# Optimization experiments

Hardware: AMD Instinct MI355X
Metric: run time of the kernel (lower is better)

Reference implementation:

```python
import jax, jax.numpy as jnp
import numpy as np

B, N, E, H, R, L, VOCAB, KINDS = 8, 4096, 524288, 128, 8, 2, 100000, 8


def setup_inputs() -> dict:
    key = jax.random.key(0)
    ks = jax.random.split(key, 12)
    concept_ids = jax.random.randint(ks[0], (B, N), 1, VOCAB)  # avoid padding_idx 0
    kind_ids = jax.random.randint(ks[1], (B, N), 0, KINDS)
    node_mask = jnp.ones((B, N), dtype=jnp.int32)
    # edges constrained within each batch block (module assumes per-subgraph edges)
    e_batch = jax.random.randint(ks[2], (E,), 0, B)
    src = e_batch * N + jax.random.randint(ks[3], (E,), 0, N)
    dst = e_batch * N + jax.random.randint(ks[4], (E,), 0, N)
    edge_index = jnp.stack([src, dst], axis=0)
    edge_type = jax.random.randint(ks[5], (E,), 0, R)
    s = 0.02
    concept_emb = jax.random.normal(ks[6], (VOCAB, H), jnp.float32) * s
    concept_emb = concept_emb.at[0].set(0.0)  # padding_idx=0
    kind_emb = jax.random.normal(ks[7], (KINDS, H), jnp.float32) * s
    proj_W = jax.random.normal(ks[8], (H, H), jnp.float32) * s
    proj_b = jnp.zeros((H,), jnp.float32)
    self_W = jax.random.normal(ks[9], (L, H, H), jnp.float32) * s
    self_b = jnp.zeros((L, H), jnp.float32)
    rel_W = jax.random.normal(ks[10], (L, R, H, H), jnp.float32) * s
    return dict(pkg_node_concept_ids=concept_ids, pkg_node_kind_ids=kind_ids,
                pkg_node_mask=node_mask, pkg_edge_index=edge_index,
                pkg_edge_type=edge_type, concept_emb=concept_emb, kind_emb=kind_emb,
                proj_W=proj_W, proj_b=proj_b, self_W=self_W, self_b=self_b, rel_W=rel_W)


def reference(pkg_node_concept_ids, pkg_node_kind_ids, pkg_node_mask,
              pkg_edge_index, pkg_edge_type, concept_emb, kind_emb,
              proj_W, proj_b, self_W, self_b, rel_W):
    b, n = pkg_node_concept_ids.shape
    num_nodes = b * n
    # input embedding + projection (dropout = identity in eval)
    x = concept_emb[pkg_node_concept_ids] + kind_emb[pkg_node_kind_ids]  # [B,N,H]
    x = jnp.einsum('bnh,gh->bng', x, proj_W) + proj_b
    x = x.reshape(num_nodes, -1)  # packed node states [B*N, H]
    src, dst = pkg_edge_index[0], pkg_edge_index[1]
    deg = jax.ops.segment_sum(jnp.ones_like(src, dtype=x.dtype), dst,
                              num_segments=num_nodes)[:, None]
    deg = jnp.maximum(deg, 1.0)
    n_layers, n_rel = rel_W.shape[0], rel_W.shape[1]
    for l in range(n_layers):
        xs = x[src]  # [E,H] gather
        msgs = jnp.zeros_like(xs)
        for r in range(n_rel):
            msgs = msgs + jnp.where((pkg_edge_type == r)[:, None],
                                    xs @ rel_W[l, r].T, 0.0)
        agg = jax.ops.segment_sum(msgs, dst, num_segments=num_nodes) / deg
        x = jax.nn.relu(x @ self_W[l].T + self_b[l] + agg)
    out = x.reshape(b, n, -1) * pkg_node_mask[..., None].astype(x.dtype)
    return out
```

## Files before the change

kernel.cpp:

```cpp
#include <hip/hip_runtime.h>
#include <hip/hip_bf16.h>

#define NODES 32768
#define HD 128
#define NE 524288
#define NR 8

typedef unsigned int u32;
typedef unsigned short u16;
typedef __attribute__((ext_vector_type(8))) short bf16x8;
typedef __attribute__((ext_vector_type(4))) float f32x4;

#define XH_OFF   (0u)
#define XL_OFF   (8u<<20)
#define Y_OFF    (16u<<20)
#define Z_OFF    (80u<<20)
#define ADJ_OFF  (96u<<20)
#define RP_OFF   (98u<<20)
#define CUR_OFF  ((98u<<20)+(256u<<10))
#define BSUM_OFF ((98u<<20)+(512u<<10))
#define BP_OFF   ((98u<<20)+(640u<<10))

#define BP_LAYER 294912

__device__ __forceinline__ float bflo(u32 u){ union{u32 i;float f;}c; c.i=u<<16; return c.f; }
__device__ __forceinline__ float bfhi(u32 u){ union{u32 i;float f;}c; c.i=u&0xffff0000u; return c.f; }
__device__ __forceinline__ u16 f2bf(float f){
  u32 u=__float_as_uint(f);
  u32 r=u + 0x7fffu + ((u>>16)&1u);
  return (u16)(r>>16);
}
__device__ __forceinline__ float bf2f(u16 h){ return __uint_as_float(((u32)h)<<16); }

__device__ __forceinline__ void gl_lds16(const void* g, void* l){
  __builtin_amdgcn_global_load_lds((const __attribute__((address_space(1))) u32*)g,
                                   (__attribute__((address_space(3))) u32*)l, 16, 0, 0);
}

__device__ __forceinline__ void fma64(const float* At, const float* Wt,
                                      int mq, int gq, float acc[8][4])
{
#pragma unroll 8
  for(int kk=0;kk<64;kk++){
    const float4 a0=*(const float4*)&At[kk*68+mq*8];
    const float4 a1=*(const float4*)&At[kk*68+mq*8+4];
    const float4 w =*(const float4*)&Wt[kk*132+gq*4];
    float av[8]={a0.x,a0.y,a0.z,a0.w,a1.x,a1.y,a1.z,a1.w};
#pragma unroll
    for(int i=0;i<8;i++){
      acc[i][0]=fmaf(av[i],w.x,acc[i][0]);
      acc[i][1]=fmaf(av[i],w.y,acc[i][1]);
      acc[i][2]=fmaf(av[i],w.z,acc[i][2]);
      acc[i][3]=fmaf(av[i],w.w,acc[i][3]);
    }
  }
}

__global__ __launch_bounds__(256) void embed_gemm(
    const int* __restrict__ cid, const int* __restrict__ kid,
    const float* __restrict__ cemb, const float* __restrict__ kemb,
    const float* __restrict__ pW, const float* __restrict__ pb,
    u16* __restrict__ xh, u16* __restrict__ xl)
{
  __shared__ float At[64*68];
  __shared__ float Wt[64*132];
  const int tid=threadIdx.x;
  const int d0=blockIdx.x*64;
  const int mq=tid>>5, gq=tid&31;
  float acc[8][4];
#pragma unroll
  for(int i=0;i<8;i++){ acc[i][0]=0.f; acc[i][1]=0.f; acc[i][2]=0.f; acc[i][3]=0.f; }

  for(int c=0;c<2;c++){
    const int h0=c*64;
    __syncthreads();
    { int m=tid>>2; int hh=(tid&3)*16;
      int ci=cid[d0+m], ki=kid[d0+m];
      const float* cp=cemb+(size_t)ci*HD+h0+hh;
      const float* kp=kemb+(size_t)ki*HD+h0+hh;
      float* ap=&At[hh*68+m];
#pragma unroll
      for(int j=0;j<16;j+=4){
        float4 a=*(const float4*)(cp+j);
        float4 b=*(const float4*)(kp+j);
        ap[(j+0)*68]=a.x+b.x; ap[(j+1)*68]=a.y+b.y;
        ap[(j+2)*68]=a.z+b.z; ap[(j+3)*68]=a.w+b.w;
      }
    }
    { int g=tid>>1; int hh=(tid&1)*32;
      const float* wp=pW+(size_t)g*HD+h0+hh;
      float* wl=&Wt[hh*132+g];
#pragma unroll
      for(int j=0;j<32;j+=4){
        float4 w=*(const float4*)(wp+j);
        wl[(j+0)*132]=w.x; wl[(j+1)*132]=w.y; wl[(j+2)*132]=w.z; wl[(j+3)*132]=w.w;
      }
    }
    __syncthreads();
    fma64(At,Wt,mq,gq,acc);
  }
  const float4 bias=*(const float4*)&pb[gq*4];
#pragma unroll
  for(int i=0;i<8;i++){
    int m=d0+mq*8+i;
    float v[4]={acc[i][0]+bias.x,acc[i][1]+bias.y,acc[i][2]+bias.z,acc[i][3]+bias.w};
    u16 hb[4], lb[4];
#pragma unroll
    for(int j=0;j<4;j++){ hb[j]=f2bf(v[j]); lb[j]=f2bf(v[j]-bf2f(hb[j])); }
    uint2 hv={(u32)hb[0]|((u32)hb[1]<<16),(u32)hb[2]|((u32)hb[3]<<16)};
    uint2 lv={(u32)lb[0]|((u32)lb[1]<<16),(u32)lb[2]|((u32)lb[3]<<16)};
    *(uint2*)&xh[(size_t)m*HD+gq*4]=hv;
    *(uint2*)&xl[(size_t)m*HD+gq*4]=lv;
  }
}

__global__ void prep_w(const float* __restrict__ rW, const float* __restrict__ sW,
                       u16* __restrict__ Bp)
{
  int idx=blockIdx.x*256+threadIdx.x;
  int l=idx/147456;
  int rem=idx%147456;
  int t=rem>>14;
  int kn=rem&16383;
  int k=kn>>7, n=kn&127;
  float w;
  if(t<8) w=rW[(((size_t)l*NR+t)*HD+n)*HD+k];
  else    w=sW[((size_t)l*HD+n)*HD+k];
  u16* base=Bp+(size_t)l*BP_LAYER+(size_t)t*32768;
  int kc=k>>6, kin=k&63, ks=kin>>5, q=(kin>>3)&3, j=kin&7;
  size_t off=((size_t)(kc*2+ks)*128+n)*32+q*8+j;
  u16 hb=f2bf(w);
  u16 lb=f2bf(w-bf2f(hb));
  base[off]=hb;
  base[off+16384]=lb;
}

__global__ void count_deg(const int* __restrict__ dst, u32* __restrict__ cnt){
  int e=blockIdx.x*256+threadIdx.x;
  atomicAdd(&cnt[dst[e]],1u);
}

__global__ void scan1(const u32* __restrict__ cnt, u32* __restrict__ rp, u32* __restrict__ bsum){
  __shared__ u32 sh[256];
  int t=threadIdx.x; int base=blockIdx.x*256;
  u32 v=cnt[base+t]; sh[t]=v; __syncthreads();
  for(int off=1;off<256;off<<=1){
    u32 tv=(t>=off)?sh[t-off]:0u; __syncthreads();
    sh[t]+=tv; __syncthreads();
  }
  rp[base+t]=sh[t]-v;
  if(t==255) bsum[blockIdx.x]=sh[255];
}

__global__ void scan2(u32* __restrict__ bsum, u32* __restrict__ rp){
  __shared__ u32 sh[128];
  int t=threadIdx.x;
  u32 v=bsum[t]; sh[t]=v; __syncthreads();
  for(int off=1;off<128;off<<=1){
    u32 tv=(t>=off)?sh[t-off]:0u; __syncthreads();
    sh[t]+=tv; __syncthreads();
  }
  bsum[t]=sh[t]-v;
  if(t==0) rp[NODES]=NE;
}

__global__ void scan3(u32* __restrict__ rp, const u32* __restrict__ bsum){
  int i=blockIdx.x*256+threadIdx.x;
  rp[i]+=bsum[blockIdx.x];
}

__global__ void scatter_edges(const int* __restrict__ src, const int* __restrict__ dst,
                              const int* __restrict__ et, const u32* __restrict__ rp,
                              u32* __restrict__ cur, u32* __restrict__ adj){
  int e=blockIdx.x*256+threadIdx.x;
  int d=dst[e];
  u32 pos=atomicAdd(&cur[d],1u);
  adj[rp[d]+pos]=(u32)src[e] | ((u32)et[e]<<16);
}

__global__ __launch_bounds__(256) void gemm_y(
    const u16* __restrict__ xhi, const u16* __restrict__ xlo,
    const u16* __restrict__ Bt, u16* __restrict__ y, float* __restrict__ z)
{
  __shared__ u16 Atile[128*64];
  const int tid=threadIdx.x;
  const int wave=tid>>6, lane=tid&63;
  const int wm=wave>>1, wn=wave&1;
  const int q=lane>>4;
  const int d0=blockIdx.x*128;
  const int t=blockIdx.y;
  const u16* Btile=Bt+(size_t)t*32768;

  f32x4 acc[4][4];
#pragma unroll
  for(int a=0;a<4;a++)
#pragma unroll
    for(int b=0;b<4;b++) acc[a][b]=(f32x4){0.f,0.f,0.f,0.f};

  const int st_row_in = lane>>3;
  const int st_gj = (lane&7) ^ (lane>>3);

#pragma unroll
  for(int part=0;part<2;part++){
    const u16* xs = part? xlo : xhi;
    const int nseg = part? 1 : 2;
    for(int c=0;c<2;c++){
      __syncthreads();
#pragma unroll
      for(int i_=0;i_<4;i_++){
        int r_=wave*32+i_*8+st_row_in;
        const u16* g_=xs+(size_t)(d0+r_)*HD+c*64+st_gj*8;
        gl_lds16(g_, &Atile[(wave*32+i_*8)*64]);
      }
      __syncthreads();
      bf16x8 afr[2][4];
#pragma unroll
      for(int ks=0;ks<2;ks++)
#pragma unroll
        for(int tm=0;tm<4;tm++){
          int m=wm*64+tm*16+(lane&15);
          afr[ks][tm]=*(const bf16x8*)&Atile[m*64+(((ks*4)+q)^(m&7))*8];
        }
      for(int s=0;s<nseg;s++){
        const u16* Bb=Btile + s*16384;
#pragma unroll
        for(int ks=0;ks<2;ks++){
#pragma unroll
          for(int tn=0;tn<4;tn++){
            int n=wn*64+tn*16+(lane&15);
            bf16x8 bfr=*(const bf16x8*)&Bb[((size_t)(c*2+ks)*128+n)*32+q*8];
#pragma unroll
            for(int tm=0;tm<4;tm++)
              acc[tm][tn]=__builtin_amdgcn_mfma_f32_16x16x32_bf16(afr[ks][tm],bfr,acc[tm][tn],0,0,0);
          }
        }
      }
    }
  }

#pragma unroll
  for(int tn=0;tn<4;tn++){
    int n=wn*64+tn*16+(lane&15);
#pragma unroll
    for(int tm=0;tm<4;tm++){
      int rbase=d0+wm*64+tm*16+q*4;
#pragma unroll
      for(int r=0;r<4;r++){
        int m=rbase+r;
        if(t<8) y[((size_t)t*NODES+m)*HD+n]=f2bf(acc[tm][tn][r]);
        else    z[(size_t)m*HD+n]=acc[tm][tn][r];
      }
    }
  }
}

__global__ __launch_bounds__(256) void gather_combine(
    const u32* __restrict__ y, const float* __restrict__ z,
    const u32* __restrict__ adj, const u32* __restrict__ rp,
    const float* __restrict__ sb, const int* __restrict__ mask,
    u32* __restrict__ xh, u32* __restrict__ xl, float* __restrict__ outf, int last)
{
  const int wave=threadIdx.x>>6, lane=threadIdx.x&63;
  const int node=blockIdx.x*4+wave;
  const int beg=(int)rp[node], end=(int)rp[node+1];
  float a0=0.f, a1=0.f;
  int e=beg;
  for(; e+4<=end; e+=4){
    u32 q0=adj[e], q1=adj[e+1], q2=adj[e+2], q3=adj[e+3];
    u32 v0=y[((size_t)(q0>>16)*NODES+(q0&0x7fffu))*64+lane];
    u32 v1=y[((size_t)(q1>>16)*NODES+(q1&0x7fffu))*64+lane];
    u32 v2=y[((size_t)(q2>>16)*NODES+(q2&0x7fffu))*64+lane];
    u32 v3=y[((size_t)(q3>>16)*NODES+(q3&0x7fffu))*64+lane];
    a0+=bflo(v0)+bflo(v1)+bflo(v2)+bflo(v3);
    a1+=bfhi(v0)+bfhi(v1)+bfhi(v2)+bfhi(v3);
  }
  for(; e<end; ++e){
    u32 qq=adj[e];
    u32 v=y[((size_t)(qq>>16)*NODES+(qq&0x7fffu))*64+lane];
    a0+=bflo(v); a1+=bfhi(v);
  }
  float inv=1.f/fmaxf((float)(end-beg),1.f);
  float2 zz=*(const float2*)&z[(size_t)node*HD+2*lane];
  float2 bb=*(const float2*)&sb[2*lane];
  float v0=fmaxf(zz.x+a0*inv+bb.x,0.f);
  float v1=fmaxf(zz.y+a1*inv+bb.y,0.f);
  if(last){
    float mk=(float)mask[node];
    float2 o={v0*mk,v1*mk};
    *(float2*)&outf[(size_t)node*HD+2*lane]=o;
  } else {
    u16 h0=f2bf(v0), h1=f2bf(v1);
    u16 l0=f2bf(v0-bf2f(h0)), l1=f2bf(v1-bf2f(h1));
    xh[(size_t)node*64+lane]=(u32)h0|((u32)h1<<16);
    xl[(size_t)node*64+lane]=(u32)l0|((u32)l1<<16);
  }
}

extern "C" void kernel_launch(void* const* d_in, const int* in_sizes, int n_in,
                              void* d_out, int out_size, void* d_ws, size_t ws_size,
                              hipStream_t stream)
{
  (void)in_sizes; (void)n_in; (void)out_size; (void)ws_size;
  const int*   cid =(const int*)  d_in[0];
  const int*   kid =(const int*)  d_in[1];
  const int*   mask=(const int*)  d_in[2];
  const int*   ei  =(const int*)  d_in[3];
  const int*   et  =(const int*)  d_in[4];
  const float* cemb=(const float*)d_in[5];
  const float* kemb=(const float*)d_in[6];
  const float* pW  =(const float*)d_in[7];
  const float* pb  =(const float*)d_in[8];
  const float* sW  =(const float*)d_in[9];
  const float* sb  =(const float*)d_in[10];
  const float* rW  =(const float*)d_in[11];
  float* out=(float*)d_out;
  char*  ws =(char*)d_ws;

  u16* xh =(u16*)(ws+XH_OFF);
  u16* xl =(u16*)(ws+XL_OFF);
  u16* y  =(u16*)(ws+Y_OFF);
  float* z=(float*)(ws+Z_OFF);
  u32* adj =(u32*)(ws+ADJ_OFF);
  u32* rp  =(u32*)(ws+RP_OFF);
  u32* cur =(u32*)(ws+CUR_OFF);
  u32* bsum=(u32*)(ws+BSUM_OFF);
  u16* Bp  =(u16*)(ws+BP_OFF);
  const int* srcA=ei;
  const int* dstA=ei+NE;

  hipMemsetAsync(cur,0,NODES*sizeof(u32),stream);
  prep_w<<<1152,256,0,stream>>>(rW,sW,Bp);
  embed_gemm<<<NODES/64,256,0,stream>>>(cid,kid,cemb,kemb,pW,pb,xh,xl);
  count_deg<<<NE/256,256,0,stream>>>(dstA,cur);
  scan1<<<NODES/256,256,0,stream>>>(cur,rp,bsum);
  scan2<<<1,128,0,stream>>>(bsum,rp);
  scan3<<<NODES/256,256,0,stream>>>(rp,bsum);
  hipMemsetAsync(cur,0,NODES*sizeof(u32),stream);
  scatter_edges<<<NE/256,256,0,stream>>>(srcA,dstA,et,rp,cur,adj);

  gemm_y<<<dim3(NODES/128,9),256,0,stream>>>(xh,xl,Bp,y,z);
  gather_combine<<<NODES/4,256,0,stream>>>((const u32*)y,z,adj,rp,sb,mask,(u32*)xh,(u32*)xl,out,0);
  gemm_y<<<dim3(NODES/128,9),256,0,stream>>>(xh,xl,Bp+BP_LAYER,y,z);
  gather_combine<<<NODES/4,256,0,stream>>>((const u32*)y,z,adj,rp,sb+HD,mask,(u32*)xh,(u32*)xl,out,1);
}
```

Baseline: 360.9 us.

## Load node tile once and loop all relation transforms inside gemm_y

```diff
diff --git a/kernel.cpp b/kernel.cpp
--- a/kernel.cpp
+++ b/kernel.cpp
@@ -178,77 +178,112 @@
   adj[rp[d]+pos]=(u32)src[e] | ((u32)et[e]<<16);
 }
 
-__global__ __launch_bounds__(256) void gemm_y(
+__global__ __launch_bounds__(256,2) void gemm_y(
     const u16* __restrict__ xhi, const u16* __restrict__ xlo,
     const u16* __restrict__ Bt, u16* __restrict__ y, float* __restrict__ z)
 {
-  __shared__ u16 Atile[128*64];
+  __shared__ u16 Atile[4][64*64];
   const int tid=threadIdx.x;
   const int wave=tid>>6, lane=tid&63;
-  const int wm=wave>>1, wn=wave&1;
   const int q=lane>>4;
-  const int d0=blockIdx.x*128;
-  const int t=blockIdx.y;
-  const u16* Btile=Bt+(size_t)t*32768;
-
-  f32x4 acc[4][4];
-#pragma unroll
-  for(int a=0;a<4;a++)
-#pragma unroll
-    for(int b=0;b<4;b++) acc[a][b]=(f32x4){0.f,0.f,0.f,0.f};
-
-  const int st_row_in = lane>>3;
-  const int st_gj = (lane&7) ^ (lane>>3);
+  const int d0=blockIdx.x*64;
+
+  const int st_row_in=lane>>3;
+  const int st_gj=(lane&7)^(lane>>3);
 
 #pragma unroll
   for(int part=0;part<2;part++){
     const u16* xs = part? xlo : xhi;
-    const int nseg = part? 1 : 2;
+#pragma unroll
     for(int c=0;c<2;c++){
-      __syncthreads();
-#pragma unroll
-      for(int i_=0;i_<4;i_++){
-        int r_=wave*32+i_*8+st_row_in;
-        const u16* g_=xs+(size_t)(d0+r_)*HD+c*64+st_gj*8;
-        gl_lds16(g_, &Atile[(wave*32+i_*8)*64]);
-      }
-      __syncthreads();
-      bf16x8 afr[2][4];
-#pragma unroll
-      for(int ks=0;ks<2;ks++)
+#pragma unroll
+      for(int i_=0;i_<2;i_++){
+        int r_=wave*16+i_*8+st_row_in;
+        const u16* g_=xs+(size_t)(d0+r_)*HD + c*64 + st_gj*8;
+        gl_lds16(g_, &Atile[part*2+c][(wave*16+i_*8)*64]);
+      }
+    }
+  }
+  __syncthreads();
+
+  bf16x8 ahi[2][2][4];
+#pragma unroll
+  for(int c=0;c<2;c++)
+#pragma unroll
+    for(int ks=0;ks<2;ks++)
+#pragma unroll
+      for(int tm=0;tm<4;tm++){
+        int m=tm*16+(lane&15);
+        ahi[c][ks][tm]=*(const bf16x8*)&Atile[c][m*64+(((ks*4)+q)^(m&7))*8];
+      }
+
+  const int nbase=wave*32+(lane&15);
+
+  for(int t=0;t<9;t++){
+    const u16* Btile=Bt+(size_t)t*32768;
+    f32x4 acc[4][2];
+#pragma unroll
+    for(int tm=0;tm<4;tm++){ acc[tm][0]=(f32x4){0.f,0.f,0.f,0.f}; acc[tm][1]=(f32x4){0.f,0.f,0.f,0.f}; }
+
+#pragma unroll
+    for(int s=0;s<2;s++){
+      const u16* Bb=Btile+s*16384;
+#pragma unroll
+      for(int c=0;c<2;c++)
+#pragma unroll
+        for(int ks=0;ks<2;ks++)
+#pragma unroll
+          for(int tn=0;tn<2;tn++){
+            bf16x8 bfr=*(const bf16x8*)&Bb[((size_t)(c*2+ks)*128+nbase+tn*16)*32+q*8];
+#pragma unroll
+            for(int tm=0;tm<4;tm++)
+              acc[tm][tn]=__builtin_amdgcn_mfma_f32_16x16x32_bf16(ahi[c][ks][tm],bfr,acc[tm][tn],0,0,0);
+          }
+    }
+#pragma unroll
+    for(int c=0;c<2;c++)
+#pragma unroll
+      for(int ks=0;ks<2;ks++){
+        bf16x8 alo[4];
 #pragma unroll
         for(int tm=0;tm<4;tm++){
-          int m=wm*64+tm*16+(lane&15);
-          afr[ks][tm]=*(const bf16x8*)&Atile[m*64+(((ks*4)+q)^(m&7))*8];
+          int m=tm*16+(lane&15);
+          alo[tm]=*(const bf16x8*)&Atile[2+c][m*64+(((ks*4)+q)^(m&7))*8];
         }
-      for(int s=0;s<nseg;s++){
-        const u16* Bb=Btile + s*16384;
-#pragma unroll
-        for(int ks=0;ks<2;ks++){
-#pragma unroll
-          for(int tn=0;tn<4;tn++){
-            int n=wn*64+tn*16+(lane&15);
-            bf16x8 bfr=*(const bf16x8*)&Bb[((size_t)(c*2+ks)*128+n)*32+q*8];
-#pragma unroll
-            for(int tm=0;tm<4;tm++)
-              acc[tm][tn]=__builtin_amdgcn_mfma_f32_16x16x32_bf16(afr[ks][tm],bfr,acc[tm][tn],0,0,0);
-          }
+#pragma unroll
+        for(int tn=0;tn<2;tn++){
+          bf16x8 bfr=*(const bf16x8*)&Btile[((size_t)(c*2+ks)*128+nbase+tn*16)*32+q*8];
+#pragma unroll
+          for(int tm=0;tm<4;tm++)
+            acc[tm][tn]=__builtin_amdgcn_mfma_f32_16x16x32_bf16(alo[tm],bfr,acc[tm][tn],0,0,0);
         }
       }
-    }
-  }
-
-#pragma unroll
-  for(int tn=0;tn<4;tn++){
-    int n=wn*64+tn*16+(lane&15);
-#pragma unroll
-    for(int tm=0;tm<4;tm++){
-      int rbase=d0+wm*64+tm*16+q*4;
-#pragma unroll
-      for(int r=0;r<4;r++){
-        int m=rbase+r;
-        if(t<8) y[((size_t)t*NODES+m)*HD+n]=f2bf(acc[tm][tn][r]);
-        else    z[(size_t)m*HD+n]=acc[tm][tn][r];
+
+    if(t<8){
+      u16* yt=y+((size_t)t*NODES+d0)*HD;
+#pragma unroll
+      for(int tn=0;tn<2;tn++){
+        int n=nbase+tn*16;
+#pragma unroll
+        for(int tm=0;tm<4;tm++){
+          int rbase=tm*16+q*4;
+#pragma unroll
+          for(int r=0;r<4;r++)
+            yt[(size_t)(rbase+r)*HD+n]=f2bf(acc[tm][tn][r]);
+        }
+      }
+    } else {
+      float* zt=z+(size_t)d0*HD;
+#pragma unroll
+      for(int tn=0;tn<2;tn++){
+        int n=nbase+tn*16;
+#pragma unroll
+        for(int tm=0;tm<4;tm++){
+          int rbase=tm*16+q*4;
+#pragma unroll
+          for(int r=0;r<4;r++)
+            zt[(size_t)(rbase+r)*HD+n]=acc[tm][tn][r];
+        }
       }
     }
   }
@@ -265,14 +300,14 @@
   const int beg=(int)rp[node], end=(int)rp[node+1];
   float a0=0.f, a1=0.f;
   int e=beg;
-  for(; e+4<=end; e+=4){
-    u32 q0=adj[e], q1=adj[e+1], q2=adj[e+2], q3=adj[e+3];
-    u32 v0=y[((size_t)(q0>>16)*NODES+(q0&0x7fffu))*64+lane];
-    u32 v1=y[((size_t)(q1>>16)*NODES+(q1&0x7fffu))*64+lane];
-    u32 v2=y[((size_t)(q2>>16)*NODES+(q2&0x7fffu))*64+lane];
-    u32 v3=y[((size_t)(q3>>16)*NODES+(q3&0x7fffu))*64+lane];
-    a0+=bflo(v0)+bflo(v1)+bflo(v2)+bflo(v3);
-    a1+=bfhi(v0)+bfhi(v1)+bfhi(v2)+bfhi(v3);
+  for(; e+8<=end; e+=8){
+    u32 qv[8], vv[8];
+#pragma unroll
+    for(int i=0;i<8;i++) qv[i]=adj[e+i];
+#pragma unroll
+    for(int i=0;i<8;i++) vv[i]=y[((size_t)(qv[i]>>16)*NODES+(qv[i]&0x7fffu))*64+lane];
+#pragma unroll
+    for(int i=0;i<8;i++){ a0+=bflo(vv[i]); a1+=bfhi(vv[i]); }
   }
   for(; e<end; ++e){
     u32 qq=adj[e];
@@ -338,8 +373,8 @@
   hipMemsetAsync(cur,0,NODES*sizeof(u32),stream);
   scatter_edges<<<NE/256,256,0,stream>>>(srcA,dstA,et,rp,cur,adj);
 
-  gemm_y<<<dim3(NODES/128,9),256,0,stream>>>(xh,xl,Bp,y,z);
+  gemm_y<<<NODES/64,256,0,stream>>>(xh,xl,Bp,y,z);
   gather_combine<<<NODES/4,256,0,stream>>>((const u32*)y,z,adj,rp,sb,mask,(u32*)xh,(u32*)xl,out,0);
-  gemm_y<<<dim3(NODES/128,9),256,0,stream>>>(xh,xl,Bp+BP_LAYER,y,z);
+  gemm_y<<<NODES/64,256,0,stream>>>(xh,xl,Bp+BP_LAYER,y,z);
   gather_combine<<<NODES/4,256,0,stream>>>((const u32*)y,z,adj,rp,sb+HD,mask,(u32*)xh,(u32*)xl,out,1);
 }
```

Result: slower. 453.2 us (+25.6%).
